# Kernel tuning notes

Measured on AMD Instinct MI355X. Metric: run time of the kernel, lower is better.

Reference implementation:

```python
import jax, jax.numpy as jnp
import numpy as np

D_MODEL = 512
D_AUX = 64
B, N = 8, 2048


def setup_inputs() -> dict:
    key = jax.random.key(0)
    ks = jax.random.split(key, 12)
    lim = 1.0 / np.sqrt(D_MODEL)  # torch Linear default init scale
    inp = {
        "x": jax.random.normal(ks[0], (B, N, D_MODEL), dtype=jnp.float32),
        "query_aux": jax.random.normal(ks[1], (B, N, D_AUX), dtype=jnp.float32),
        "key_aux": jax.random.normal(ks[2], (B, N, D_AUX), dtype=jnp.float32),
        "adjacency_mask": jax.random.randint(ks[3], (B, N, N), 0, 2, dtype=jnp.int32),
        "merge_coefficients": jnp.float32(0.3),
        "Wq": jax.random.uniform(ks[4], (D_MODEL, D_MODEL), jnp.float32, -lim, lim),
        "bq": jax.random.uniform(ks[5], (D_MODEL,), jnp.float32, -lim, lim),
        "Wk": jax.random.uniform(ks[6], (D_MODEL, D_MODEL), jnp.float32, -lim, lim),
        "bk": jax.random.uniform(ks[7], (D_MODEL,), jnp.float32, -lim, lim),
        "Wv": jax.random.uniform(ks[8], (D_MODEL, D_MODEL), jnp.float32, -lim, lim),
        "bv": jax.random.uniform(ks[9], (D_MODEL,), jnp.float32, -lim, lim),
        "threshold": jnp.float32(0.5),
    }
    return inp


def reference(x, query_aux, key_aux, adjacency_mask, merge_coefficients,
              Wq, bq, Wk, bk, Wv, bv, threshold):
    d_model = x.shape[-1]
    d_aux = key_aux.shape[-1]
    scale = jnp.asarray(d_model, x.dtype) ** 0.5
    scale_aux = jnp.asarray(d_aux, x.dtype) ** 0.5

    q = x @ Wq.T + bq  # [B,N,D]
    k = x @ Wk.T + bk
    v = x @ Wv.T + bv

    scores = jnp.einsum('bnd,bmd->bnm', q, k) / scale  # [B,N,N]
    scores_aux = jnp.einsum('bnd,bmd->bnm', query_aux, key_aux) / scale_aux

    # data-dependent merge: where aux score nonzero AND score above learned threshold
    merge_mask = (scores_aux != 0) & (scores > threshold)
    merged = (1.0 - merge_coefficients) * scores + merge_coefficients * scores_aux
    scores = jnp.where(merge_mask, merged, scores)

    mask_value = jnp.finfo(scores.dtype).min
    scores = jnp.where(adjacency_mask == 0, mask_value, scores)

    weights = jax.nn.softmax(scores, axis=-1)
    return jnp.einsum('bnm,bmd->bnd', weights, v)
```

## Files before the change

### kernel.cpp

```cpp
#include <hip/hip_runtime.h>
#include <cstdint>

#define SEQ    2048
#define DM     512
#define DAUX   64

typedef _Float16 f16;
typedef __attribute__((ext_vector_type(2))) _Float16 f16x2;
typedef __attribute__((ext_vector_type(4))) _Float16 f16x4;
typedef __attribute__((ext_vector_type(8))) _Float16 f16x8;
typedef __attribute__((ext_vector_type(4))) float fx4;
typedef __attribute__((ext_vector_type(16))) float fx16;

__device__ __forceinline__ void g2l16(const void* g, void* l) {
  __builtin_amdgcn_global_load_lds(
      (__attribute__((address_space(1))) void*)const_cast<void*>(g),
      (__attribute__((address_space(3))) void*)l, 16, 0, 0);
}

__device__ __forceinline__ void stage32(const f16* __restrict__ g0, int stride,
                                        f16* lds, int t) {
#pragma unroll
  for (int p = 0; p < 2; ++p) {
    int L = p * 256 + t;
    int row = L >> 2;
    int jp = L & 3;
    int jl = jp ^ ((row >> 1) & 3);
    g2l16(g0 + (size_t)row * stride + jl * 8, lds + L * 8);
  }
}
__device__ __forceinline__ f16x8 frag32(const f16* lds, int row, int kq) {
  int jp = (kq >> 3) ^ ((row >> 1) & 3);
  return *(const f16x8*)(lds + row * 32 + jp * 8);
}

__device__ __forceinline__ void stage64(const f16* __restrict__ g0, int stride,
                                        f16* lds, int t) {
#pragma unroll
  for (int p = 0; p < 4; ++p) {
    int L = p * 256 + t;
    int row = L >> 3;
    int jp = L & 7;
    int jl = jp ^ (row & 7);
    g2l16(g0 + (size_t)row * stride + jl * 8, lds + L * 8);
  }
}
__device__ __forceinline__ f16x8 frag64(const f16* lds, int row, int kq) {
  int jp = (kq >> 3) ^ (row & 7);
  return *(const f16x8*)(lds + row * 64 + jp * 8);
}

__device__ __forceinline__ void chunk3_32(const f16* Ah, const f16* Al,
                                          const f16* Bh, const f16* Bl,
                                          fx16 acc[2][2], int wm, int wn, int lane) {
  const int r31 = lane & 31;
  const int kq = (lane >> 5) * 8;
#pragma unroll
  for (int k0 = 0; k0 < 32; k0 += 16) {
    f16x8 ah[2], al[2];
#pragma unroll
    for (int it = 0; it < 2; ++it) {
      int row = wm * 64 + it * 32 + r31;
      ah[it] = frag32(Ah, row, k0 + kq);
      al[it] = frag32(Al, row, k0 + kq);
    }
#pragma unroll
    for (int jt = 0; jt < 2; ++jt) {
      int col = wn * 64 + jt * 32 + r31;
      f16x8 bh = frag32(Bh, col, k0 + kq);
      f16x8 bl = frag32(Bl, col, k0 + kq);
#pragma unroll
      for (int it = 0; it < 2; ++it) {
        acc[it][jt] = __builtin_amdgcn_mfma_f32_32x32x16_f16(ah[it], bh, acc[it][jt], 0, 0, 0);
        acc[it][jt] = __builtin_amdgcn_mfma_f32_32x32x16_f16(ah[it], bl, acc[it][jt], 0, 0, 0);
        acc[it][jt] = __builtin_amdgcn_mfma_f32_32x32x16_f16(al[it], bh, acc[it][jt], 0, 0, 0);
      }
    }
  }
}

__device__ __forceinline__ void chunk1_64(const f16* A, const f16* B,
                                          fx16 acc[2][2], int wm, int wn, int lane) {
  const int r31 = lane & 31;
  const int kq = (lane >> 5) * 8;
#pragma unroll
  for (int k0 = 0; k0 < 64; k0 += 16) {
    f16x8 a[2];
#pragma unroll
    for (int it = 0; it < 2; ++it)
      a[it] = frag64(A, wm * 64 + it * 32 + r31, k0 + kq);
#pragma unroll
    for (int jt = 0; jt < 2; ++jt) {
      f16x8 b = frag64(B, wn * 64 + jt * 32 + r31, k0 + kq);
#pragma unroll
      for (int it = 0; it < 2; ++it)
        acc[it][jt] = __builtin_amdgcn_mfma_f32_32x32x16_f16(a[it], b, acc[it][jt], 0, 0, 0);
    }
  }
}

__global__ __launch_bounds__(256) void convert_split(
    const float* __restrict__ x, const float* __restrict__ Wq,
    const float* __restrict__ Wk, const float* __restrict__ Wv,
    f16* __restrict__ xh, f16* __restrict__ xl,
    f16* __restrict__ Wh, f16* __restrict__ Wl) {
  int idx = blockIdx.x * 256 + threadIdx.x;
  const float* src; f16* dh; f16* dl; size_t off;
  if (idx < 2097152) { src = x; off = (size_t)idx; dh = xh; dl = xl; }
  else {
    int rr = idx - 2097152;
    int w = rr >> 16, o = rr & 65535;
    src = (w == 0) ? Wq : (w == 1) ? Wk : Wv;
    off = (size_t)o;
    dh = Wh + (size_t)w * 262144; dl = Wl + (size_t)w * 262144;
  }
  float4 v = ((const float4*)src)[off];
  float vv[4] = {v.x, v.y, v.z, v.w};
  f16x4 hv, lv;
#pragma unroll
  for (int i = 0; i < 4; ++i) {
    float s = vv[i] * 32.0f;
    f16 hi = (f16)s;
    hv[i] = hi;
    lv[i] = (f16)(s - (float)hi);
  }
  *(f16x4*)(dh + off * 4) = hv;
  *(f16x4*)(dl + off * 4) = lv;
}

__global__ __launch_bounds__(256) void qkv_mfma(
    const f16* __restrict__ xh, const f16* __restrict__ xl,
    const f16* __restrict__ Wh, const f16* __restrict__ Wl,
    const float* __restrict__ bq, const float* __restrict__ bk, const float* __restrict__ bv,
    f16* __restrict__ qh, f16* __restrict__ ql,
    f16* __restrict__ kh, f16* __restrict__ kl,
    f16* __restrict__ vt) {
  __shared__ __align__(16) f16 sm[32768];
  const int t = threadIdx.x;
  const int i0 = blockIdx.x * 128, j0 = blockIdx.y * 128, z = blockIdx.z;
  const f16* WhZ = Wh + (size_t)z * 262144;
  const f16* WlZ = Wl + (size_t)z * 262144;
  const int lane = t & 63, wave = t >> 6;
  const int wm = wave >> 1, wn = wave & 1;
  const int r31 = lane & 31, half = lane >> 5;
  fx16 acc[2][2] = {};
  const f16* xhB = xh + (size_t)i0 * DM;
  const f16* xlB = xl + (size_t)i0 * DM;
  const f16* WhB = WhZ + (size_t)j0 * DM;
  const f16* WlB = WlZ + (size_t)j0 * DM;
  if (z < 2) {
    stage32(xhB, DM, sm, t);
    stage32(xlB, DM, sm + 4096, t);
    stage32(WhB, DM, sm + 8192, t);
    stage32(WlB, DM, sm + 12288, t);
    __syncthreads();
    for (int c = 0; c < 16; ++c) {
      f16* cur = sm + (c & 1) * 16384;
      if (c < 15) {
        f16* nxt = sm + ((c + 1) & 1) * 16384;
        int d0 = (c + 1) * 32;
        stage32(xhB + d0, DM, nxt, t);
        stage32(xlB + d0, DM, nxt + 4096, t);
        stage32(WhB + d0, DM, nxt + 8192, t);
        stage32(WlB + d0, DM, nxt + 12288, t);
      }
      chunk3_32(cur, cur + 4096, cur + 8192, cur + 12288, acc, wm, wn, lane);
      if (c < 15) __syncthreads();
    }
  } else {
    stage64(xhB, DM, sm, t);
    stage64(WhB, DM, sm + 8192, t);
    __syncthreads();
    for (int c = 0; c < 8; ++c) {
      f16* cur = sm + (c & 1) * 16384;
      if (c < 7) {
        f16* nxt = sm + ((c + 1) & 1) * 16384;
        int d0 = (c + 1) * 64;
        stage64(xhB + d0, DM, nxt, t);
        stage64(WhB + d0, DM, nxt + 8192, t);
      }
      chunk1_64(cur, cur + 8192, acc, wm, wn, lane);
      if (c < 7) __syncthreads();
    }
  }
  const float* bias = (z == 0) ? bq : (z == 1) ? bk : bv;
  if (z < 2) {
    f16* oh = z ? kh : qh;  f16* ol = z ? kl : ql;
#pragma unroll
    for (int it = 0; it < 2; ++it)
#pragma unroll
      for (int jt = 0; jt < 2; ++jt) {
        int j = j0 + wn * 64 + jt * 32 + r31;
        float bj = bias[j];
#pragma unroll
        for (int r = 0; r < 16; ++r) {
          int ib = i0 + wm * 64 + it * 32 + (r & 3) + 8 * (r >> 2) + 4 * half;
          float val = acc[it][jt][r] * (1.0f / 1024.0f) + bj;
          float s = val * 32.0f;
          f16 hi = (f16)s;
          oh[(size_t)ib * DM + j] = hi;
          ol[(size_t)ib * DM + j] = (f16)(s - (float)hi);
        }
      }
  } else {
#pragma unroll
    for (int it = 0; it < 2; ++it)
#pragma unroll
      for (int jt = 0; jt < 2; ++jt) {
        int j = j0 + wn * 64 + jt * 32 + r31;
        float bj = bias[j];
#pragma unroll
        for (int q4 = 0; q4 < 4; ++q4) {
          int ib = i0 + wm * 64 + it * 32 + 8 * q4 + 4 * half;
          int bb = ib >> 11, nb = ib & 2047;
          f16x4 hv;
#pragma unroll
          for (int g = 0; g < 4; ++g)
            hv[g] = (f16)(acc[it][jt][q4 * 4 + g] * (1.0f / 1024.0f) + bj);
          *(f16x4*)(vt + ((size_t)(bb * DM + j)) * SEQ + nb) = hv;
        }
      }
  }
}

__global__ __launch_bounds__(256) void scores_mfma(
    const f16* __restrict__ qh, const f16* __restrict__ ql,
    const f16* __restrict__ kh, const f16* __restrict__ kl,
    const float* __restrict__ qa, const float* __restrict__ ka,
    const int* __restrict__ adj,
    const float* __restrict__ mc_p, const float* __restrict__ thr_p,
    f16* __restrict__ S16) {
  __shared__ __align__(16) f16 sm[32768];
  const int t = threadIdx.x;
  const int n0 = blockIdx.x * 128, m0 = blockIdx.y * 128, b = blockIdx.z;
  const int lane = t & 63, wave = t >> 6;
  const int wm = wave >> 1, wn = wave & 1;
  const int r31 = lane & 31, half = lane >> 5;
  const int kq = half * 8;

  const f16* qhB = qh + ((size_t)b * SEQ + n0) * DM;
  const f16* qlB = ql + ((size_t)b * SEQ + n0) * DM;
  const f16* khB = kh + ((size_t)b * SEQ + m0) * DM;
  const f16* klB = kl + ((size_t)b * SEQ + m0) * DM;

  stage32(qhB, DM, sm, t);
  stage32(qlB, DM, sm + 4096, t);
  stage32(khB, DM, sm + 8192, t);
  stage32(klB, DM, sm + 12288, t);

  f16* QAl = sm + 16384;
  f16* KAl = sm + 24576;
  const float* QAb = qa + ((size_t)b * SEQ + n0) * DAUX;
  const float* KAb = ka + ((size_t)b * SEQ + m0) * DAUX;
#pragma unroll
  for (int p = 0; p < 4; ++p) {
    int L8 = p * 256 + t;
    int row = L8 >> 3, jb = L8 & 7;
    int c8 = jb * 8;
    int jp = jb ^ (row & 7);
    float4 u0 = *(const float4*)(QAb + (size_t)row * DAUX + c8);
    float4 u1 = *(const float4*)(QAb + (size_t)row * DAUX + c8 + 4);
    f16x8 hq = {(f16)u0.x,(f16)u0.y,(f16)u0.z,(f16)u0.w,(f16)u1.x,(f16)u1.y,(f16)u1.z,(f16)u1.w};
    *(f16x8*)(QAl + row * 64 + jp * 8) = hq;
    float4 w0 = *(const float4*)(KAb + (size_t)row * DAUX + c8);
    float4 w1 = *(const float4*)(KAb + (size_t)row * DAUX + c8 + 4);
    f16x8 hk = {(f16)w0.x,(f16)w0.y,(f16)w0.z,(f16)w0.w,(f16)w1.x,(f16)w1.y,(f16)w1.z,(f16)w1.w};
    *(f16x8*)(KAl + row * 64 + jp * 8) = hk;
  }
  __syncthreads();

  f16x2 sax2[2][2][8];
  {
    fx16 aacc[2][2] = {};
#pragma unroll
    for (int k0 = 0; k0 < 64; k0 += 16) {
      f16x8 qaf[2];
#pragma unroll
      for (int it = 0; it < 2; ++it)
        qaf[it] = frag64(QAl, wm * 64 + it * 32 + r31, k0 + kq);
#pragma unroll
      for (int jt = 0; jt < 2; ++jt) {
        f16x8 kaf = frag64(KAl, wn * 64 + jt * 32 + r31, k0 + kq);
#pragma unroll
        for (int it = 0; it < 2; ++it)
          aacc[it][jt] = __builtin_amdgcn_mfma_f32_32x32x16_f16(qaf[it], kaf, aacc[it][jt], 0, 0, 0);
      }
    }
#pragma unroll
    for (int it = 0; it < 2; ++it)
#pragma unroll
      for (int jt = 0; jt < 2; ++jt)
#pragma unroll
        for (int r = 0; r < 16; ++r)
          sax2[it][jt][r >> 1][r & 1] = (f16)aacc[it][jt][r];
  }
  __syncthreads();

  fx16 acc[2][2] = {};
  for (int c = 0; c < 16; ++c) {
    f16* cur = sm + (c & 1) * 16384;
    if (c < 15) {
      f16* nxt = sm + ((c + 1) & 1) * 16384;
      int d0 = (c + 1) * 32;
      stage32(qhB + d0, DM, nxt, t);
      stage32(qlB + d0, DM, nxt + 4096, t);
      stage32(khB + d0, DM, nxt + 8192, t);
      stage32(klB + d0, DM, nxt + 12288, t);
    }
    chunk3_32(cur, cur + 4096, cur + 8192, cur + 12288, acc, wm, wn, lane);
    if (c < 15) __syncthreads();
  }

  const float mc = *mc_p, thr = *thr_p;
  const float invC = 1.0f / (1024.0f * 22.62741699796952f);
#pragma unroll
  for (int it = 0; it < 2; ++it)
#pragma unroll
    for (int jt = 0; jt < 2; ++jt) {
      int col = m0 + wn * 64 + jt * 32 + r31;
#pragma unroll
      for (int r = 0; r < 16; ++r) {
        int row = n0 + wm * 64 + it * 32 + (r & 3) + 8 * (r >> 2) + 4 * half;
        size_t rbase = ((size_t)b * SEQ + row) * SEQ;
        float s = acc[it][jt][r] * invC;
        float sa = (float)sax2[it][jt][r >> 1][r & 1] * 0.125f;
        if (sa != 0.0f && s > thr) s = (1.0f - mc) * s + mc * sa;
        if (adj[rbase + col] == 0) s = -65504.0f;
        S16[rbase + col] = (f16)s;
      }
    }
}

__global__ __launch_bounds__(256) void softmax_p(
    f16* __restrict__ S16, float* __restrict__ rowsum) {
  const int wv = threadIdx.x >> 6, ln = threadIdx.x & 63;
  const size_t row = (size_t)blockIdx.x * 4 + wv;
  f16* Sr = S16 + row * SEQ;
  f16x8 v[4];
  float vals[32];
#pragma unroll
  for (int j = 0; j < 4; ++j) {
    v[j] = *(const f16x8*)(Sr + j * 512 + ln * 8);
#pragma unroll
    for (int i = 0; i < 8; ++i) vals[j * 8 + i] = (float)v[j][i];
  }
  float m = vals[0];
#pragma unroll
  for (int i = 1; i < 32; ++i) m = fmaxf(m, vals[i]);
#pragma unroll
  for (int off = 1; off < 64; off <<= 1) m = fmaxf(m, __shfl_xor(m, off, 64));
  float z = 0.f;
  f16x8 p16[4];
#pragma unroll
  for (int j = 0; j < 4; ++j)
#pragma unroll
    for (int i = 0; i < 8; ++i) {
      f16 p = (f16)(__expf(vals[j * 8 + i] - m) * 1024.0f);
      p16[j][i] = p;
      z += (float)p;
    }
#pragma unroll
  for (int off = 1; off < 64; off <<= 1) z += __shfl_xor(z, off, 64);
  if (ln == 0) rowsum[row] = z;
#pragma unroll
  for (int j = 0; j < 4; ++j)
    *(f16x8*)(Sr + j * 512 + ln * 8) = p16[j];
}

__global__ __launch_bounds__(256) void pv_mfma(
    const f16* __restrict__ P16, const f16* __restrict__ vt,
    const float* __restrict__ rowsum, float* __restrict__ O) {
  __shared__ __align__(16) f16 sm[32768];
  const int t = threadIdx.x;
  const int n0 = blockIdx.x * 128, d0 = blockIdx.y * 128, b = blockIdx.z;
  const int lane = t & 63, wave = t >> 6;
  const int wm = wave >> 1, wn = wave & 1;
  const int r31 = lane & 31, half = lane >> 5;
  fx16 acc[2][2] = {};
  const f16* Pb = P16 + ((size_t)b * SEQ + n0) * SEQ;
  const f16* Vb = vt + ((size_t)b * DM + d0) * SEQ;
  stage64(Pb, SEQ, sm, t);
  stage64(Vb, SEQ, sm + 8192, t);
  __syncthreads();
  for (int c = 0; c < 32; ++c) {
    f16* cur = sm + (c & 1) * 16384;
    if (c < 31) {
      f16* nxt = sm + ((c + 1) & 1) * 16384;
      int m0 = (c + 1) * 64;
      stage64(Pb + m0, SEQ, nxt, t);
      stage64(Vb + m0, SEQ, nxt + 8192, t);
    }
    chunk1_64(cur, cur + 8192, acc, wm, wn, lane);
    if (c < 31) __syncthreads();
  }
#pragma unroll
  for (int it = 0; it < 2; ++it)
#pragma unroll
    for (int jt = 0; jt < 2; ++jt) {
      int d = d0 + wn * 64 + jt * 32 + r31;
#pragma unroll
      for (int r = 0; r < 16; ++r) {
        int n = n0 + wm * 64 + it * 32 + (r & 3) + 8 * (r >> 2) + 4 * half;
        float inv = 1.0f / rowsum[(size_t)b * SEQ + n];
        O[((size_t)b * SEQ + n) * DM + d] = acc[it][jt][r] * inv;
      }
    }
}

extern "C" void kernel_launch(void* const* d_in, const int* in_sizes, int n_in,
                              void* d_out, int out_size, void* d_ws, size_t ws_size,
                              hipStream_t stream) {
  const float* x   = (const float*)d_in[0];
  const float* qa  = (const float*)d_in[1];
  const float* ka  = (const float*)d_in[2];
  const int*   adj = (const int*)d_in[3];
  const float* mc  = (const float*)d_in[4];
  const float* Wq  = (const float*)d_in[5];
  const float* bq  = (const float*)d_in[6];
  const float* Wk  = (const float*)d_in[7];
  const float* bk  = (const float*)d_in[8];
  const float* Wv  = (const float*)d_in[9];
  const float* bv  = (const float*)d_in[10];
  const float* thr = (const float*)d_in[11];
  float* out = (float*)d_out;

  f16* qh  = (f16*)d_ws;
  f16* ql  = qh + 8388608;
  f16* kh  = ql + 8388608;
  f16* kl  = kh + 8388608;
  f16* vt  = kl + 8388608;
  f16* S16 = vt + 8388608;
  float* rowsum = (float*)(S16 + 33554432);
  f16* xh = S16;
  f16* xl = xh + 8388608;
  f16* Wh = xl + 8388608;
  f16* Wl = Wh + 786432;

  convert_split<<<8960, 256, 0, stream>>>(x, Wq, Wk, Wv, xh, xl, Wh, Wl);
  qkv_mfma<<<dim3(128, 4, 3), 256, 0, stream>>>(xh, xl, Wh, Wl, bq, bk, bv,
                                                qh, ql, kh, kl, vt);
  scores_mfma<<<dim3(16, 16, 8), 256, 0, stream>>>(qh, ql, kh, kl, qa, ka, adj,
                                                   mc, thr, S16);
  softmax_p<<<4096, 256, 0, stream>>>(S16, rowsum);
  pv_mfma<<<dim3(16, 4, 8), 256, 0, stream>>>(S16, vt, rowsum, out);
}
```

Measured before the change: 498.0 us.

## Halve LDS tiles for higher occupancy and split PV reduction across two blocks

```diff
diff --git a/kernel.cpp b/kernel.cpp
--- a/kernel.cpp
+++ b/kernel.cpp
@@ -18,6 +18,17 @@
       (__attribute__((address_space(3))) void*)l, 16, 0, 0);
 }
 
+__device__ __forceinline__ void stage16(const f16* __restrict__ g0, int stride,
+                                        f16* lds, int t) {
+  int row = t >> 1, jp = t & 1;
+  int jl = jp ^ ((row >> 2) & 1);
+  g2l16(g0 + (size_t)row * stride + jl * 8, lds + t * 8);
+}
+__device__ __forceinline__ f16x8 frag16(const f16* lds, int row, int kq) {
+  int jp = (kq >> 3) ^ ((row >> 2) & 1);
+  return *(const f16x8*)(lds + row * 16 + jp * 8);
+}
+
 __device__ __forceinline__ void stage32(const f16* __restrict__ g0, int stride,
                                         f16* lds, int t) {
 #pragma unroll
@@ -34,64 +45,46 @@
   return *(const f16x8*)(lds + row * 32 + jp * 8);
 }
 
-__device__ __forceinline__ void stage64(const f16* __restrict__ g0, int stride,
-                                        f16* lds, int t) {
-#pragma unroll
-  for (int p = 0; p < 4; ++p) {
-    int L = p * 256 + t;
-    int row = L >> 3;
-    int jp = L & 7;
-    int jl = jp ^ (row & 7);
-    g2l16(g0 + (size_t)row * stride + jl * 8, lds + L * 8);
-  }
-}
-__device__ __forceinline__ f16x8 frag64(const f16* lds, int row, int kq) {
-  int jp = (kq >> 3) ^ (row & 7);
-  return *(const f16x8*)(lds + row * 64 + jp * 8);
-}
-
-__device__ __forceinline__ void chunk3_32(const f16* Ah, const f16* Al,
+
+__device__ __forceinline__ void chunk3_16(const f16* Ah, const f16* Al,
                                           const f16* Bh, const f16* Bl,
                                           fx16 acc[2][2], int wm, int wn, int lane) {
   const int r31 = lane & 31;
   const int kq = (lane >> 5) * 8;
-#pragma unroll
-  for (int k0 = 0; k0 < 32; k0 += 16) {
-    f16x8 ah[2], al[2];
+  f16x8 ah[2], al[2];
+#pragma unroll
+  for (int it = 0; it < 2; ++it) {
+    int row = wm * 64 + it * 32 + r31;
+    ah[it] = frag16(Ah, row, kq);
+    al[it] = frag16(Al, row, kq);
+  }
+#pragma unroll
+  for (int jt = 0; jt < 2; ++jt) {
+    int col = wn * 64 + jt * 32 + r31;
+    f16x8 bh = frag16(Bh, col, kq);
+    f16x8 bl = frag16(Bl, col, kq);
 #pragma unroll
     for (int it = 0; it < 2; ++it) {
-      int row = wm * 64 + it * 32 + r31;
-      ah[it] = frag32(Ah, row, k0 + kq);
-      al[it] = frag32(Al, row, k0 + kq);
-    }
-#pragma unroll
-    for (int jt = 0; jt < 2; ++jt) {
-      int col = wn * 64 + jt * 32 + r31;
-      f16x8 bh = frag32(Bh, col, k0 + kq);
-      f16x8 bl = frag32(Bl, col, k0 + kq);
-#pragma unroll
-      for (int it = 0; it < 2; ++it) {
-        acc[it][jt] = __builtin_amdgcn_mfma_f32_32x32x16_f16(ah[it], bh, acc[it][jt], 0, 0, 0);
-        acc[it][jt] = __builtin_amdgcn_mfma_f32_32x32x16_f16(ah[it], bl, acc[it][jt], 0, 0, 0);
-        acc[it][jt] = __builtin_amdgcn_mfma_f32_32x32x16_f16(al[it], bh, acc[it][jt], 0, 0, 0);
-      }
-    }
-  }
-}
-
-__device__ __forceinline__ void chunk1_64(const f16* A, const f16* B,
+      acc[it][jt] = __builtin_amdgcn_mfma_f32_32x32x16_f16(ah[it], bh, acc[it][jt], 0, 0, 0);
+      acc[it][jt] = __builtin_amdgcn_mfma_f32_32x32x16_f16(ah[it], bl, acc[it][jt], 0, 0, 0);
+      acc[it][jt] = __builtin_amdgcn_mfma_f32_32x32x16_f16(al[it], bh, acc[it][jt], 0, 0, 0);
+    }
+  }
+}
+
+__device__ __forceinline__ void chunk1_32(const f16* A, const f16* B,
                                           fx16 acc[2][2], int wm, int wn, int lane) {
   const int r31 = lane & 31;
   const int kq = (lane >> 5) * 8;
 #pragma unroll
-  for (int k0 = 0; k0 < 64; k0 += 16) {
+  for (int k0 = 0; k0 < 32; k0 += 16) {
     f16x8 a[2];
 #pragma unroll
     for (int it = 0; it < 2; ++it)
-      a[it] = frag64(A, wm * 64 + it * 32 + r31, k0 + kq);
+      a[it] = frag32(A, wm * 64 + it * 32 + r31, k0 + kq);
 #pragma unroll
     for (int jt = 0; jt < 2; ++jt) {
-      f16x8 b = frag64(B, wn * 64 + jt * 32 + r31, k0 + kq);
+      f16x8 b = frag32(B, wn * 64 + jt * 32 + r31, k0 + kq);
 #pragma unroll
       for (int it = 0; it < 2; ++it)
         acc[it][jt] = __builtin_amdgcn_mfma_f32_32x32x16_f16(a[it], b, acc[it][jt], 0, 0, 0);
@@ -128,14 +121,14 @@
   *(f16x4*)(dl + off * 4) = lv;
 }
 
-__global__ __launch_bounds__(256) void qkv_mfma(
+__global__ __launch_bounds__(256, 4) void qkv_mfma(
     const f16* __restrict__ xh, const f16* __restrict__ xl,
     const f16* __restrict__ Wh, const f16* __restrict__ Wl,
     const float* __restrict__ bq, const float* __restrict__ bk, const float* __restrict__ bv,
     f16* __restrict__ qh, f16* __restrict__ ql,
     f16* __restrict__ kh, f16* __restrict__ kl,
     f16* __restrict__ vt) {
-  __shared__ __align__(16) f16 sm[32768];
+  __shared__ __align__(16) f16 sm[16384];
   const int t = threadIdx.x;
   const int i0 = blockIdx.x * 128, j0 = blockIdx.y * 128, z = blockIdx.z;
   const f16* WhZ = Wh + (size_t)z * 262144;
@@ -149,38 +142,38 @@
   const f16* WhB = WhZ + (size_t)j0 * DM;
   const f16* WlB = WlZ + (size_t)j0 * DM;
   if (z < 2) {
+    stage16(xhB, DM, sm, t);
+    stage16(xlB, DM, sm + 2048, t);
+    stage16(WhB, DM, sm + 4096, t);
+    stage16(WlB, DM, sm + 6144, t);
+    __syncthreads();
+    for (int c = 0; c < 32; ++c) {
+      f16* cur = sm + (c & 1) * 8192;
+      if (c < 31) {
+        f16* nxt = sm + ((c + 1) & 1) * 8192;
+        int d0 = (c + 1) * 16;
+        stage16(xhB + d0, DM, nxt, t);
+        stage16(xlB + d0, DM, nxt + 2048, t);
+        stage16(WhB + d0, DM, nxt + 4096, t);
+        stage16(WlB + d0, DM, nxt + 6144, t);
+      }
+      chunk3_16(cur, cur + 2048, cur + 4096, cur + 6144, acc, wm, wn, lane);
+      if (c < 31) __syncthreads();
+    }
+  } else {
     stage32(xhB, DM, sm, t);
-    stage32(xlB, DM, sm + 4096, t);
-    stage32(WhB, DM, sm + 8192, t);
-    stage32(WlB, DM, sm + 12288, t);
+    stage32(WhB, DM, sm + 4096, t);
     __syncthreads();
     for (int c = 0; c < 16; ++c) {
-      f16* cur = sm + (c & 1) * 16384;
+      f16* cur = sm + (c & 1) * 8192;
       if (c < 15) {
-        f16* nxt = sm + ((c + 1) & 1) * 16384;
+        f16* nxt = sm + ((c + 1) & 1) * 8192;
         int d0 = (c + 1) * 32;
         stage32(xhB + d0, DM, nxt, t);
-        stage32(xlB + d0, DM, nxt + 4096, t);
-        stage32(WhB + d0, DM, nxt + 8192, t);
-        stage32(WlB + d0, DM, nxt + 12288, t);
-      }
-      chunk3_32(cur, cur + 4096, cur + 8192, cur + 12288, acc, wm, wn, lane);
+        stage32(WhB + d0, DM, nxt + 4096, t);
+      }
+      chunk1_32(cur, cur + 4096, acc, wm, wn, lane);
       if (c < 15) __syncthreads();
-    }
-  } else {
-    stage64(xhB, DM, sm, t);
-    stage64(WhB, DM, sm + 8192, t);
-    __syncthreads();
-    for (int c = 0; c < 8; ++c) {
-      f16* cur = sm + (c & 1) * 16384;
-      if (c < 7) {
-        f16* nxt = sm + ((c + 1) & 1) * 16384;
-        int d0 = (c + 1) * 64;
-        stage64(xhB + d0, DM, nxt, t);
-        stage64(WhB + d0, DM, nxt + 8192, t);
-      }
-      chunk1_64(cur, cur + 8192, acc, wm, wn, lane);
-      if (c < 7) __syncthreads();
     }
   }
   const float* bias = (z == 0) ? bq : (z == 1) ? bk : bv;
@@ -223,14 +216,14 @@
   }
 }
 
-__global__ __launch_bounds__(256) void scores_mfma(
+__global__ __launch_bounds__(256, 4) void scores_mfma(
     const f16* __restrict__ qh, const f16* __restrict__ ql,
     const f16* __restrict__ kh, const f16* __restrict__ kl,
     const float* __restrict__ qa, const float* __restrict__ ka,
     const int* __restrict__ adj,
     const float* __restrict__ mc_p, const float* __restrict__ thr_p,
     f16* __restrict__ S16) {
-  __shared__ __align__(16) f16 sm[32768];
+  __shared__ __align__(16) f16 sm[16384];
   const int t = threadIdx.x;
   const int n0 = blockIdx.x * 128, m0 = blockIdx.y * 128, b = blockIdx.z;
   const int lane = t & 63, wave = t >> 6;
@@ -243,44 +236,34 @@
   const f16* khB = kh + ((size_t)b * SEQ + m0) * DM;
   const f16* klB = kl + ((size_t)b * SEQ + m0) * DM;
 
-  stage32(qhB, DM, sm, t);
-  stage32(qlB, DM, sm + 4096, t);
-  stage32(khB, DM, sm + 8192, t);
-  stage32(klB, DM, sm + 12288, t);
-
-  f16* QAl = sm + 16384;
-  f16* KAl = sm + 24576;
-  const float* QAb = qa + ((size_t)b * SEQ + n0) * DAUX;
-  const float* KAb = ka + ((size_t)b * SEQ + m0) * DAUX;
-#pragma unroll
-  for (int p = 0; p < 4; ++p) {
-    int L8 = p * 256 + t;
-    int row = L8 >> 3, jb = L8 & 7;
-    int c8 = jb * 8;
-    int jp = jb ^ (row & 7);
-    float4 u0 = *(const float4*)(QAb + (size_t)row * DAUX + c8);
-    float4 u1 = *(const float4*)(QAb + (size_t)row * DAUX + c8 + 4);
-    f16x8 hq = {(f16)u0.x,(f16)u0.y,(f16)u0.z,(f16)u0.w,(f16)u1.x,(f16)u1.y,(f16)u1.z,(f16)u1.w};
-    *(f16x8*)(QAl + row * 64 + jp * 8) = hq;
-    float4 w0 = *(const float4*)(KAb + (size_t)row * DAUX + c8);
-    float4 w1 = *(const float4*)(KAb + (size_t)row * DAUX + c8 + 4);
-    f16x8 hk = {(f16)w0.x,(f16)w0.y,(f16)w0.z,(f16)w0.w,(f16)w1.x,(f16)w1.y,(f16)w1.z,(f16)w1.w};
-    *(f16x8*)(KAl + row * 64 + jp * 8) = hk;
-  }
-  __syncthreads();
+  stage16(qhB, DM, sm, t);
+  stage16(qlB, DM, sm + 2048, t);
+  stage16(khB, DM, sm + 4096, t);
+  stage16(klB, DM, sm + 6144, t);
 
   f16x2 sax2[2][2][8];
   {
     fx16 aacc[2][2] = {};
+    const float* QAb = qa + ((size_t)b * SEQ + n0) * DAUX;
+    const float* KAb = ka + ((size_t)b * SEQ + m0) * DAUX;
 #pragma unroll
     for (int k0 = 0; k0 < 64; k0 += 16) {
       f16x8 qaf[2];
 #pragma unroll
-      for (int it = 0; it < 2; ++it)
-        qaf[it] = frag64(QAl, wm * 64 + it * 32 + r31, k0 + kq);
+      for (int it = 0; it < 2; ++it) {
+        const float* p = QAb + (size_t)(wm * 64 + it * 32 + r31) * DAUX + k0 + kq;
+        float4 u0 = *(const float4*)p;
+        float4 u1 = *(const float4*)(p + 4);
+        qaf[it] = (f16x8){(f16)u0.x,(f16)u0.y,(f16)u0.z,(f16)u0.w,
+                          (f16)u1.x,(f16)u1.y,(f16)u1.z,(f16)u1.w};
+      }
 #pragma unroll
       for (int jt = 0; jt < 2; ++jt) {
-        f16x8 kaf = frag64(KAl, wn * 64 + jt * 32 + r31, k0 + kq);
+        const float* p = KAb + (size_t)(wn * 64 + jt * 32 + r31) * DAUX + k0 + kq;
+        float4 w0 = *(const float4*)p;
+        float4 w1 = *(const float4*)(p + 4);
+        f16x8 kaf = {(f16)w0.x,(f16)w0.y,(f16)w0.z,(f16)w0.w,
+                     (f16)w1.x,(f16)w1.y,(f16)w1.z,(f16)w1.w};
 #pragma unroll
         for (int it = 0; it < 2; ++it)
           aacc[it][jt] = __builtin_amdgcn_mfma_f32_32x32x16_f16(qaf[it], kaf, aacc[it][jt], 0, 0, 0);
@@ -297,18 +280,18 @@
   __syncthreads();
 
   fx16 acc[2][2] = {};
-  for (int c = 0; c < 16; ++c) {
-    f16* cur = sm + (c & 1) * 16384;
-    if (c < 15) {
-      f16* nxt = sm + ((c + 1) & 1) * 16384;
-      int d0 = (c + 1) * 32;
-      stage32(qhB + d0, DM, nxt, t);
-      stage32(qlB + d0, DM, nxt + 4096, t);
-      stage32(khB + d0, DM, nxt + 8192, t);
-      stage32(klB + d0, DM, nxt + 12288, t);
-    }
-    chunk3_32(cur, cur + 4096, cur + 8192, cur + 12288, acc, wm, wn, lane);
-    if (c < 15) __syncthreads();
+  for (int c = 0; c < 32; ++c) {
+    f16* cur = sm + (c & 1) * 8192;
+    if (c < 31) {
+      f16* nxt = sm + ((c + 1) & 1) * 8192;
+      int d0 = (c + 1) * 16;
+      stage16(qhB + d0, DM, nxt, t);
+      stage16(qlB + d0, DM, nxt + 2048, t);
+      stage16(khB + d0, DM, nxt + 4096, t);
+      stage16(klB + d0, DM, nxt + 6144, t);
+    }
+    chunk3_16(cur, cur + 2048, cur + 4096, cur + 6144, acc, wm, wn, lane);
+    if (c < 31) __syncthreads();
   }
 
   const float mc = *mc_p, thr = *thr_p;
@@ -367,30 +350,32 @@
     *(f16x8*)(Sr + j * 512 + ln * 8) = p16[j];
 }
 
-__global__ __launch_bounds__(256) void pv_mfma(
+__global__ __launch_bounds__(256, 4) void pv_mfma(
     const f16* __restrict__ P16, const f16* __restrict__ vt,
     const float* __restrict__ rowsum, float* __restrict__ O) {
-  __shared__ __align__(16) f16 sm[32768];
+  __shared__ __align__(16) f16 sm[16384];
   const int t = threadIdx.x;
-  const int n0 = blockIdx.x * 128, d0 = blockIdx.y * 128, b = blockIdx.z;
+  const int n0 = blockIdx.x * 128, d0 = blockIdx.y * 128;
+  const int b = blockIdx.z >> 1;
+  const int mh = (blockIdx.z & 1) << 10;
   const int lane = t & 63, wave = t >> 6;
   const int wm = wave >> 1, wn = wave & 1;
   const int r31 = lane & 31, half = lane >> 5;
   fx16 acc[2][2] = {};
-  const f16* Pb = P16 + ((size_t)b * SEQ + n0) * SEQ;
-  const f16* Vb = vt + ((size_t)b * DM + d0) * SEQ;
-  stage64(Pb, SEQ, sm, t);
-  stage64(Vb, SEQ, sm + 8192, t);
+  const f16* Pb = P16 + ((size_t)b * SEQ + n0) * SEQ + mh;
+  const f16* Vb = vt + ((size_t)b * DM + d0) * SEQ + mh;
+  stage32(Pb, SEQ, sm, t);
+  stage32(Vb, SEQ, sm + 4096, t);
   __syncthreads();
   for (int c = 0; c < 32; ++c) {
-    f16* cur = sm + (c & 1) * 16384;
+    f16* cur = sm + (c & 1) * 8192;
     if (c < 31) {
-      f16* nxt = sm + ((c + 1) & 1) * 16384;
-      int m0 = (c + 1) * 64;
-      stage64(Pb + m0, SEQ, nxt, t);
-      stage64(Vb + m0, SEQ, nxt + 8192, t);
-    }
-    chunk1_64(cur, cur + 8192, acc, wm, wn, lane);
+      f16* nxt = sm + ((c + 1) & 1) * 8192;
+      int m0c = (c + 1) * 32;
+      stage32(Pb + m0c, SEQ, nxt, t);
+      stage32(Vb + m0c, SEQ, nxt + 4096, t);
+    }
+    chunk1_32(cur, cur + 4096, acc, wm, wn, lane);
     if (c < 31) __syncthreads();
   }
 #pragma unroll
@@ -402,7 +387,7 @@
       for (int r = 0; r < 16; ++r) {
         int n = n0 + wm * 64 + it * 32 + (r & 3) + 8 * (r >> 2) + 4 * half;
         float inv = 1.0f / rowsum[(size_t)b * SEQ + n];
-        O[((size_t)b * SEQ + n) * DM + d] = acc[it][jt][r] * inv;
+        atomicAdd(&O[((size_t)b * SEQ + n) * DM + d], acc[it][jt][r] * inv);
       }
     }
 }
@@ -442,5 +427,6 @@
   scores_mfma<<<dim3(16, 16, 8), 256, 0, stream>>>(qh, ql, kh, kl, qa, ka, adj,
                                                    mc, thr, S16);
   softmax_p<<<4096, 256, 0, stream>>>(S16, rowsum);
-  pv_mfma<<<dim3(16, 4, 8), 256, 0, stream>>>(S16, vt, rowsum, out);
-}
+  hipMemsetAsync(d_out, 0, (size_t)out_size, stream);
+  pv_mfma<<<dim3(16, 4, 16), 256, 0, stream>>>(S16, vt, rowsum, out);
+}
```

Result: slower. 756.9 us (+52.0%).

## Restructure scores kernel to 8 waves with smaller K-chunks and halved LDS

Applied to the files above, without the earlier changes.

```diff
diff --git a/kernel.cpp b/kernel.cpp
--- a/kernel.cpp
+++ b/kernel.cpp
@@ -48,6 +48,11 @@
 __device__ __forceinline__ f16x8 frag64(const f16* lds, int row, int kq) {
   int jp = (kq >> 3) ^ (row & 7);
   return *(const f16x8*)(lds + row * 64 + jp * 8);
+}
+
+__device__ __forceinline__ f16x8 frag16(const f16* lds, int row, int kq) {
+  int jp = (kq >> 3) ^ ((row >> 2) & 1);
+  return *(const f16x8*)(lds + row * 16 + jp * 8);
 }
 
 __device__ __forceinline__ void chunk3_32(const f16* Ah, const f16* Al,
@@ -223,18 +228,18 @@
   }
 }
 
-__global__ __launch_bounds__(256) void scores_mfma(
+__global__ __launch_bounds__(512, 4) void scores_mfma(
     const f16* __restrict__ qh, const f16* __restrict__ ql,
     const f16* __restrict__ kh, const f16* __restrict__ kl,
     const float* __restrict__ qa, const float* __restrict__ ka,
     const int* __restrict__ adj,
     const float* __restrict__ mc_p, const float* __restrict__ thr_p,
     f16* __restrict__ S16) {
-  __shared__ __align__(16) f16 sm[32768];
+  __shared__ __align__(16) f16 sm[16384];
   const int t = threadIdx.x;
   const int n0 = blockIdx.x * 128, m0 = blockIdx.y * 128, b = blockIdx.z;
   const int lane = t & 63, wave = t >> 6;
-  const int wm = wave >> 1, wn = wave & 1;
+  const int wm = wave >> 2, wn = wave & 3;
   const int r31 = lane & 31, half = lane >> 5;
   const int kq = half * 8;
 
@@ -243,92 +248,103 @@
   const f16* khB = kh + ((size_t)b * SEQ + m0) * DM;
   const f16* klB = kl + ((size_t)b * SEQ + m0) * DM;
 
-  stage32(qhB, DM, sm, t);
-  stage32(qlB, DM, sm + 4096, t);
-  stage32(khB, DM, sm + 8192, t);
-  stage32(klB, DM, sm + 12288, t);
-
-  f16* QAl = sm + 16384;
-  f16* KAl = sm + 24576;
-  const float* QAb = qa + ((size_t)b * SEQ + n0) * DAUX;
-  const float* KAb = ka + ((size_t)b * SEQ + m0) * DAUX;
-#pragma unroll
-  for (int p = 0; p < 4; ++p) {
-    int L8 = p * 256 + t;
-    int row = L8 >> 3, jb = L8 & 7;
-    int c8 = jb * 8;
-    int jp = jb ^ (row & 7);
-    float4 u0 = *(const float4*)(QAb + (size_t)row * DAUX + c8);
-    float4 u1 = *(const float4*)(QAb + (size_t)row * DAUX + c8 + 4);
-    f16x8 hq = {(f16)u0.x,(f16)u0.y,(f16)u0.z,(f16)u0.w,(f16)u1.x,(f16)u1.y,(f16)u1.z,(f16)u1.w};
-    *(f16x8*)(QAl + row * 64 + jp * 8) = hq;
-    float4 w0 = *(const float4*)(KAb + (size_t)row * DAUX + c8);
-    float4 w1 = *(const float4*)(KAb + (size_t)row * DAUX + c8 + 4);
-    f16x8 hk = {(f16)w0.x,(f16)w0.y,(f16)w0.z,(f16)w0.w,(f16)w1.x,(f16)w1.y,(f16)w1.z,(f16)w1.w};
-    *(f16x8*)(KAl + row * 64 + jp * 8) = hk;
-  }
+#define STAGE16Q(D0, DST)                                                      \
+  {                                                                            \
+    _Pragma("unroll")                                                          \
+    for (int p = 0; p < 2; ++p) {                                              \
+      int o = p * 512 + t;                                                     \
+      int a = o >> 8;                                                          \
+      int s = o & 255;                                                         \
+      int row = s >> 1, jp = s & 1;                                            \
+      int jl = jp ^ ((row >> 2) & 1);                                          \
+      const f16* g = (a == 0) ? qhB : (a == 1) ? qlB : (a == 2) ? khB : klB;   \
+      g2l16(g + (size_t)row * DM + (D0) + jl * 8, (DST) + a * 2048 + s * 8);   \
+    }                                                                          \
+  }
+
+  STAGE16Q(0, sm);
   __syncthreads();
 
-  f16x2 sax2[2][2][8];
+  fx16 acc[2] = {};
+  for (int c = 0; c < 32; ++c) {
+    f16* cur = sm + (c & 1) * 8192;
+    if (c < 31) {
+      f16* nxt = sm + ((c + 1) & 1) * 8192;
+      int d0 = (c + 1) * 16;
+      STAGE16Q(d0, nxt);
+    }
+    {
+      f16x8 ah[2], al[2];
+#pragma unroll
+      for (int it = 0; it < 2; ++it) {
+        int row = wm * 64 + it * 32 + r31;
+        ah[it] = frag16(cur, row, kq);
+        al[it] = frag16(cur + 2048, row, kq);
+      }
+      int col = wn * 32 + r31;
+      f16x8 bh = frag16(cur + 4096, col, kq);
+      f16x8 bl = frag16(cur + 6144, col, kq);
+#pragma unroll
+      for (int it = 0; it < 2; ++it) {
+        acc[it] = __builtin_amdgcn_mfma_f32_32x32x16_f16(ah[it], bh, acc[it], 0, 0, 0);
+        acc[it] = __builtin_amdgcn_mfma_f32_32x32x16_f16(ah[it], bl, acc[it], 0, 0, 0);
+        acc[it] = __builtin_amdgcn_mfma_f32_32x32x16_f16(al[it], bh, acc[it], 0, 0, 0);
+      }
+    }
+    if (c < 31) __syncthreads();
+  }
+  __syncthreads();
+
+  f16* QAl = sm;
+  f16* KAl = sm + 8192;
   {
-    fx16 aacc[2][2] = {};
-#pragma unroll
-    for (int k0 = 0; k0 < 64; k0 += 16) {
-      f16x8 qaf[2];
-#pragma unroll
-      for (int it = 0; it < 2; ++it)
-        qaf[it] = frag64(QAl, wm * 64 + it * 32 + r31, k0 + kq);
-#pragma unroll
-      for (int jt = 0; jt < 2; ++jt) {
-        f16x8 kaf = frag64(KAl, wn * 64 + jt * 32 + r31, k0 + kq);
-#pragma unroll
-        for (int it = 0; it < 2; ++it)
-          aacc[it][jt] = __builtin_amdgcn_mfma_f32_32x32x16_f16(qaf[it], kaf, aacc[it][jt], 0, 0, 0);
-      }
-    }
-#pragma unroll
-    for (int it = 0; it < 2; ++it)
-#pragma unroll
-      for (int jt = 0; jt < 2; ++jt)
-#pragma unroll
-        for (int r = 0; r < 16; ++r)
-          sax2[it][jt][r >> 1][r & 1] = (f16)aacc[it][jt][r];
+    const float* QAb = qa + ((size_t)b * SEQ + n0) * DAUX;
+    const float* KAb = ka + ((size_t)b * SEQ + m0) * DAUX;
+#pragma unroll
+    for (int p = 0; p < 4; ++p) {
+      int o = p * 512 + t;
+      const float* src = (p < 2) ? QAb : KAb;
+      f16* dst = (p < 2) ? QAl : KAl;
+      int s = o & 1023;
+      int row = s >> 3, jb = s & 7;
+      int jp = jb ^ (row & 7);
+      float4 u0 = *(const float4*)(src + (size_t)row * DAUX + jb * 8);
+      float4 u1 = *(const float4*)(src + (size_t)row * DAUX + jb * 8 + 4);
+      f16x8 h = {(f16)u0.x,(f16)u0.y,(f16)u0.z,(f16)u0.w,
+                 (f16)u1.x,(f16)u1.y,(f16)u1.z,(f16)u1.w};
+      *(f16x8*)(dst + row * 64 + jp * 8) = h;
+    }
   }
   __syncthreads();
 
-  fx16 acc[2][2] = {};
-  for (int c = 0; c < 16; ++c) {
-    f16* cur = sm + (c & 1) * 16384;
-    if (c < 15) {
-      f16* nxt = sm + ((c + 1) & 1) * 16384;
-      int d0 = (c + 1) * 32;
-      stage32(qhB + d0, DM, nxt, t);
-      stage32(qlB + d0, DM, nxt + 4096, t);
-      stage32(khB + d0, DM, nxt + 8192, t);
-      stage32(klB + d0, DM, nxt + 12288, t);
-    }
-    chunk3_32(cur, cur + 4096, cur + 8192, cur + 12288, acc, wm, wn, lane);
-    if (c < 15) __syncthreads();
+  fx16 aacc[2] = {};
+#pragma unroll
+  for (int k0 = 0; k0 < 64; k0 += 16) {
+    f16x8 kaf = frag64(KAl, wn * 32 + r31, k0 + kq);
+#pragma unroll
+    for (int it = 0; it < 2; ++it) {
+      f16x8 qaf = frag64(QAl, wm * 64 + it * 32 + r31, k0 + kq);
+      aacc[it] = __builtin_amdgcn_mfma_f32_32x32x16_f16(qaf, kaf, aacc[it], 0, 0, 0);
+    }
   }
 
   const float mc = *mc_p, thr = *thr_p;
   const float invC = 1.0f / (1024.0f * 22.62741699796952f);
-#pragma unroll
-  for (int it = 0; it < 2; ++it)
-#pragma unroll
-    for (int jt = 0; jt < 2; ++jt) {
-      int col = m0 + wn * 64 + jt * 32 + r31;
-#pragma unroll
-      for (int r = 0; r < 16; ++r) {
-        int row = n0 + wm * 64 + it * 32 + (r & 3) + 8 * (r >> 2) + 4 * half;
-        size_t rbase = ((size_t)b * SEQ + row) * SEQ;
-        float s = acc[it][jt][r] * invC;
-        float sa = (float)sax2[it][jt][r >> 1][r & 1] * 0.125f;
-        if (sa != 0.0f && s > thr) s = (1.0f - mc) * s + mc * sa;
-        if (adj[rbase + col] == 0) s = -65504.0f;
-        S16[rbase + col] = (f16)s;
-      }
-    }
+  const int col = m0 + wn * 32 + r31;
+#pragma unroll
+  for (int it = 0; it < 2; ++it) {
+#pragma unroll
+    for (int r = 0; r < 16; ++r) {
+      int row = n0 + wm * 64 + it * 32 + (r & 3) + 8 * (r >> 2) + 4 * half;
+      size_t rbase = ((size_t)b * SEQ + row) * SEQ;
+      float s = acc[it][r] * invC;
+      float sa = (float)(f16)aacc[it][r] * 0.125f;
+      if (sa != 0.0f && s > thr) s = (1.0f - mc) * s + mc * sa;
+      if (adj[rbase + col] == 0) s = -65504.0f;
+      S16[rbase + col] = (f16)s;
+    }
+  }
+#undef STAGE16Q
 }
 
 __global__ __launch_bounds__(256) void softmax_p(
@@ -439,7 +455,7 @@
   convert_split<<<8960, 256, 0, stream>>>(x, Wq, Wk, Wv, xh, xl, Wh, Wl);
   qkv_mfma<<<dim3(128, 4, 3), 256, 0, stream>>>(xh, xl, Wh, Wl, bq, bk, bv,
                                                 qh, ql, kh, kl, vt);
-  scores_mfma<<<dim3(16, 16, 8), 256, 0, stream>>>(qh, ql, kh, kl, qa, ka, adj,
+  scores_mfma<<<dim3(16, 16, 8), 512, 0, stream>>>(qh, ql, kh, kl, qa, ka, adj,
                                                    mc, thr, S16);
   softmax_p<<<4096, 256, 0, stream>>>(S16, rowsum);
   pv_mfma<<<dim3(16, 4, 8), 256, 0, stream>>>(S16, vt, rowsum, out);
```

Result: slower. 526.9 us (+5.8%).

## Triple-buffer scores K-loop with 16-wide chunks and explicit vmcnt waits

Applied to the files above, without the earlier changes.

```diff
diff --git a/kernel.cpp b/kernel.cpp
--- a/kernel.cpp
+++ b/kernel.cpp
@@ -18,6 +18,12 @@
       (__attribute__((address_space(3))) void*)l, 16, 0, 0);
 }
 
+#define WAITV8 { asm volatile("s_waitcnt vmcnt(8)" ::: "memory"); __builtin_amdgcn_sched_barrier(0); }
+#define WAITV4 { asm volatile("s_waitcnt vmcnt(4)" ::: "memory"); __builtin_amdgcn_sched_barrier(0); }
+#define WAITV0 { asm volatile("s_waitcnt vmcnt(0)" ::: "memory"); __builtin_amdgcn_sched_barrier(0); }
+#define WAITL0 { asm volatile("s_waitcnt lgkmcnt(0)" ::: "memory"); __builtin_amdgcn_sched_barrier(0); }
+#define BAR __builtin_amdgcn_s_barrier()
+
 __device__ __forceinline__ void stage32(const f16* __restrict__ g0, int stride,
                                         f16* lds, int t) {
 #pragma unroll
@@ -50,6 +56,26 @@
   return *(const f16x8*)(lds + row * 64 + jp * 8);
 }
 
+__device__ __forceinline__ f16x8 frag16(const f16* lds, int row, int kq) {
+  int jp = (kq >> 3) ^ ((row >> 2) & 1);
+  return *(const f16x8*)(lds + row * 16 + jp * 8);
+}
+
+__device__ __forceinline__ void stageS16(const f16* __restrict__ qhB,
+                                         const f16* __restrict__ qlB,
+                                         const f16* __restrict__ khB,
+                                         const f16* __restrict__ klB,
+                                         int d0, f16* buf, int t) {
+  int row = t >> 1, jp = t & 1;
+  int jl = jp ^ ((row >> 2) & 1);
+  size_t go = (size_t)row * DM + d0 + jl * 8;
+  int lo = t * 8;
+  g2l16(qhB + go, buf + lo);
+  g2l16(qlB + go, buf + 2048 + lo);
+  g2l16(khB + go, buf + 4096 + lo);
+  g2l16(klB + go, buf + 6144 + lo);
+}
+
 __device__ __forceinline__ void chunk3_32(const f16* Ah, const f16* Al,
                                           const f16* Bh, const f16* Bl,
                                           fx16 acc[2][2], int wm, int wn, int lane) {
@@ -75,6 +101,31 @@
         acc[it][jt] = __builtin_amdgcn_mfma_f32_32x32x16_f16(ah[it], bl, acc[it][jt], 0, 0, 0);
         acc[it][jt] = __builtin_amdgcn_mfma_f32_32x32x16_f16(al[it], bh, acc[it][jt], 0, 0, 0);
       }
+    }
+  }
+}
+
+__device__ __forceinline__ void chunk3_16w(const f16* buf, fx16 acc[2][2],
+                                           int wm, int wn, int lane) {
+  const int r31 = lane & 31;
+  const int kq = (lane >> 5) * 8;
+  f16x8 ah[2], al[2];
+#pragma unroll
+  for (int it = 0; it < 2; ++it) {
+    int row = wm * 64 + it * 32 + r31;
+    ah[it] = frag16(buf, row, kq);
+    al[it] = frag16(buf + 2048, row, kq);
+  }
+#pragma unroll
+  for (int jt = 0; jt < 2; ++jt) {
+    int col = wn * 64 + jt * 32 + r31;
+    f16x8 bh = frag16(buf + 4096, col, kq);
+    f16x8 bl = frag16(buf + 6144, col, kq);
+#pragma unroll
+    for (int it = 0; it < 2; ++it) {
+      acc[it][jt] = __builtin_amdgcn_mfma_f32_32x32x16_f16(ah[it], bh, acc[it][jt], 0, 0, 0);
+      acc[it][jt] = __builtin_amdgcn_mfma_f32_32x32x16_f16(ah[it], bl, acc[it][jt], 0, 0, 0);
+      acc[it][jt] = __builtin_amdgcn_mfma_f32_32x32x16_f16(al[it], bh, acc[it][jt], 0, 0, 0);
     }
   }
 }
@@ -230,7 +281,7 @@
     const int* __restrict__ adj,
     const float* __restrict__ mc_p, const float* __restrict__ thr_p,
     f16* __restrict__ S16) {
-  __shared__ __align__(16) f16 sm[32768];
+  __shared__ __align__(16) f16 sm[24576];
   const int t = threadIdx.x;
   const int n0 = blockIdx.x * 128, m0 = blockIdx.y * 128, b = blockIdx.z;
   const int lane = t & 63, wave = t >> 6;
@@ -242,14 +293,14 @@
   const f16* qlB = ql + ((size_t)b * SEQ + n0) * DM;
   const f16* khB = kh + ((size_t)b * SEQ + m0) * DM;
   const f16* klB = kl + ((size_t)b * SEQ + m0) * DM;
-
-  stage32(qhB, DM, sm, t);
-  stage32(qlB, DM, sm + 4096, t);
-  stage32(khB, DM, sm + 8192, t);
-  stage32(klB, DM, sm + 12288, t);
-
-  f16* QAl = sm + 16384;
-  f16* KAl = sm + 24576;
+  f16* const B0 = sm;
+  f16* const B1 = sm + 8192;
+  f16* const B2 = sm + 16384;
+
+  stageS16(qhB, qlB, khB, klB, 0, B0, t);
+
+  f16* QAl = B1;
+  f16* KAl = B2;
   const float* QAb = qa + ((size_t)b * SEQ + n0) * DAUX;
   const float* KAb = ka + ((size_t)b * SEQ + m0) * DAUX;
 #pragma unroll
@@ -267,7 +318,7 @@
     f16x8 hk = {(f16)w0.x,(f16)w0.y,(f16)w0.z,(f16)w0.w,(f16)w1.x,(f16)w1.y,(f16)w1.z,(f16)w1.w};
     *(f16x8*)(KAl + row * 64 + jp * 8) = hk;
   }
-  __syncthreads();
+  WAITL0; BAR;
 
   f16x2 sax2[2][2][8];
   {
@@ -294,22 +345,35 @@
         for (int r = 0; r < 16; ++r)
           sax2[it][jt][r >> 1][r & 1] = (f16)aacc[it][jt][r];
   }
-  __syncthreads();
+  WAITL0; BAR;
+
+  stageS16(qhB, qlB, khB, klB, 16, B1, t);
+  stageS16(qhB, qlB, khB, klB, 32, B2, t);
 
   fx16 acc[2][2] = {};
-  for (int c = 0; c < 16; ++c) {
-    f16* cur = sm + (c & 1) * 16384;
-    if (c < 15) {
-      f16* nxt = sm + ((c + 1) & 1) * 16384;
-      int d0 = (c + 1) * 32;
-      stage32(qhB + d0, DM, nxt, t);
-      stage32(qlB + d0, DM, nxt + 4096, t);
-      stage32(khB + d0, DM, nxt + 8192, t);
-      stage32(klB + d0, DM, nxt + 12288, t);
-    }
-    chunk3_32(cur, cur + 4096, cur + 8192, cur + 12288, acc, wm, wn, lane);
-    if (c < 15) __syncthreads();
-  }
+  for (int c = 0; c < 27; c += 3) {
+    WAITV8; BAR;
+    chunk3_16w(B0, acc, wm, wn, lane);
+    WAITL0; BAR;
+    stageS16(qhB, qlB, khB, klB, (c + 3) * 16, B0, t);
+
+    WAITV8; BAR;
+    chunk3_16w(B1, acc, wm, wn, lane);
+    WAITL0; BAR;
+    stageS16(qhB, qlB, khB, klB, (c + 4) * 16, B1, t);
+
+    WAITV8; BAR;
+    chunk3_16w(B2, acc, wm, wn, lane);
+    WAITL0; BAR;
+    stageS16(qhB, qlB, khB, klB, (c + 5) * 16, B2, t);
+  }
+  WAITV8; BAR; chunk3_16w(B0, acc, wm, wn, lane); WAITL0; BAR;
+  stageS16(qhB, qlB, khB, klB, 480, B0, t);
+  WAITV8; BAR; chunk3_16w(B1, acc, wm, wn, lane); WAITL0; BAR;
+  stageS16(qhB, qlB, khB, klB, 496, B1, t);
+  WAITV8; BAR; chunk3_16w(B2, acc, wm, wn, lane); WAITL0; BAR;
+  WAITV4; BAR; chunk3_16w(B0, acc, wm, wn, lane); WAITL0; BAR;
+  WAITV0; BAR; chunk3_16w(B1, acc, wm, wn, lane);
 
   const float mc = *mc_p, thr = *thr_p;
   const float invC = 1.0f / (1024.0f * 22.62741699796952f);
```

Measured after the change: 561.9 us. +12.8%, slower.
